# Kernel optimization log

Measured on AMD Instinct MI355X. Metric: run time of the kernel, lower is better.

Reference implementation:

```python
import jax, jax.numpy as jnp
import numpy as np

D_MODEL = 1024
N_HEADS = 16
D_K = D_MODEL // N_HEADS
SCALE = float(np.sqrt(D_K))


def setup_inputs() -> dict:
    key = jax.random.key(0)
    ks = jax.random.split(key, 8)
    B, S = 2, 2048
    init = 1.0 / np.sqrt(D_MODEL)
    return {
        "query": jax.random.normal(ks[0], (B, S, D_MODEL), dtype=jnp.float32),
        "key": jax.random.normal(ks[1], (B, S, D_MODEL), dtype=jnp.float32),
        "value": jax.random.normal(ks[2], (B, S, D_MODEL), dtype=jnp.float32),
        "w_q": jax.random.uniform(ks[3], (D_MODEL, D_MODEL), jnp.float32, -init, init),
        "w_k": jax.random.uniform(ks[4], (D_MODEL, D_MODEL), jnp.float32, -init, init),
        "w_v": jax.random.uniform(ks[5], (D_MODEL, D_MODEL), jnp.float32, -init, init),
        "w_o": jax.random.uniform(ks[6], (D_MODEL, D_MODEL), jnp.float32, -init, init),
        "b_o": jax.random.uniform(ks[7], (D_MODEL,), jnp.float32, -init, init),
    }


def reference(query, key, value, w_q, w_k, w_v, w_o, b_o):
    B, S, _ = query.shape
    # nn.Linear computes x @ W.T; weights stored torch-style [out, in]
    def proj(x, w):
        # [B,S,D] -> [B,H,S,Dk]
        return (x @ w.T).reshape(B, S, N_HEADS, D_K).transpose(0, 2, 1, 3)

    Q = proj(query, w_q)
    K = proj(key, w_k)
    V = proj(value, w_v)
    scores = jnp.einsum("bhqd,bhkd->bhqk", Q, K) / SCALE  # [B,H,S,S]
    attn = jax.nn.softmax(scores, axis=-1)
    out = jnp.einsum("bhqk,bhkd->bhqd", attn, V)  # [B,H,S,Dk]
    out = out.transpose(0, 2, 1, 3).reshape(B, S, D_MODEL)
    out = out @ w_o.T + b_o
    return (out, attn)
```

## Files before the change

kernel.cpp:

```cpp
#include <hip/hip_runtime.h>
#include <hip/hip_bf16.h>

typedef unsigned int u32;
typedef unsigned short u16;
using bf16x8 = __attribute__((ext_vector_type(8))) short;
using f32x4  = __attribute__((ext_vector_type(4))) float;

#define S_LEN 2048
#define DK 64
#define NH 16
#define DMODEL 1024
#define NROWS 4096

__device__ __forceinline__ u16 f2bf(float f){
  u32 u = __builtin_bit_cast(u32, f);
  u += 0x7fffu + ((u >> 16) & 1u);
  return (u16)(u >> 16);
}

__device__ __forceinline__ void gload_lds16(const u16* g, u16* l){
  __builtin_amdgcn_global_load_lds(
      (__attribute__((address_space(1))) u32*)(void*)const_cast<u16*>(g),
      (__attribute__((address_space(3))) u32*)(void*)l, 16, 0, 0);
}

#define TILE_BARRIER_VM4() do { \
  asm volatile("s_waitcnt vmcnt(4) lgkmcnt(0)" ::: "memory"); \
  __builtin_amdgcn_s_barrier(); \
  __builtin_amdgcn_sched_barrier(0); \
} while (0)

#define TILE_BARRIER_VM0() do { \
  asm volatile("s_waitcnt vmcnt(0) lgkmcnt(0)" ::: "memory"); \
  __builtin_amdgcn_s_barrier(); \
  __builtin_amdgcn_sched_barrier(0); \
} while (0)

__global__ void cvt_all(const float* __restrict__ q, const float* __restrict__ k,
                        const float* __restrict__ v, const float* __restrict__ wq,
                        const float* __restrict__ wk, const float* __restrict__ wv,
                        const float* __restrict__ wo, u16* __restrict__ ws)
{
  const int y = blockIdx.y;
  const int n4 = (y < 3) ? (NROWS*DMODEL/4) : (DMODEL*DMODEL/4);
  const int i = blockIdx.x * blockDim.x + threadIdx.x;
  if (i >= n4) return;
  const float* src = (y==0)?q:(y==1)?k:(y==2)?v:(y==3)?wq:(y==4)?wk:(y==5)?wv:wo;
  u16* dst = ws + ((y < 3) ? (size_t)y*(NROWS*DMODEL)
                           : (size_t)3*(NROWS*DMODEL) + (size_t)(y-3)*(DMODEL*DMODEL));
  float4 val = reinterpret_cast<const float4*>(src)[i];
  ushort4 o;
  o.x = f2bf(val.x); o.y = f2bf(val.y); o.z = f2bf(val.z); o.w = f2bf(val.w);
  reinterpret_cast<ushort4*>(dst)[i] = o;
}

template<bool OUTGEMM>
__global__ __launch_bounds__(256)
void gemm_mha(const u16* __restrict__ Abase, const u16* __restrict__ Bbase,
              u16* __restrict__ Qh, u16* __restrict__ Kh, u16* __restrict__ Vt,
              float* __restrict__ Out, const float* __restrict__ bias)
{
  __shared__ u16 smem[32768];
  u16* As = smem;
  u16* Bs = smem + 16384;

  const int tid  = threadIdx.x;
  const int lane = tid & 63;
  const int wid  = tid >> 6;
  const int lo = lane & 15, hi = lane >> 4;
  const int z = OUTGEMM ? 0 : blockIdx.z;
  const int m0 = blockIdx.x * 128;
  const int n0 = blockIdx.y * 128;
  const u16* ga = Abase + (size_t)z * (NROWS*DMODEL)  + (size_t)m0 * DMODEL;
  const u16* gb = Bbase + (size_t)z * (DMODEL*DMODEL) + (size_t)n0 * DMODEL;

  const int wm = (wid >> 1) * 64;
  const int wn = (wid & 1) * 64;

  f32x4 acc[4][4] = {};

  auto stage = [&](int buf, int kt){
    const u16* a = ga + kt * 64;
    const u16* b = gb + kt * 64;
    #pragma unroll
    for (int i = 0; i < 4; ++i){
      const int chunk = i*256 + tid;
      const int row = chunk >> 3, c8 = chunk & 7;
      gload_lds16(a + (size_t)row*DMODEL + c8*8, &As[buf*8192 + (i*256 + wid*64)*8]);
      gload_lds16(b + (size_t)row*DMODEL + c8*8, &Bs[buf*8192 + (i*256 + wid*64)*8]);
    }
  };

  stage(0, 0);
  __syncthreads();

  for (int t = 0; t < DMODEL/64; ++t){
    const int buf = t & 1;
    if (t + 1 < DMODEL/64) stage(buf ^ 1, t + 1);
    const u16* as = &As[buf*8192];
    const u16* bs = &Bs[buf*8192];
    #pragma unroll
    for (int ks = 0; ks < 2; ++ks){
      bf16x8 af[4], bfr[4];
      #pragma unroll
      for (int i = 0; i < 4; ++i){
        af[i]  = *reinterpret_cast<const bf16x8*>(&as[(wm + i*16 + lo)*64 + ks*32 + hi*8]);
        bfr[i] = *reinterpret_cast<const bf16x8*>(&bs[(wn + i*16 + lo)*64 + ks*32 + hi*8]);
      }
      #pragma unroll
      for (int mi = 0; mi < 4; ++mi)
        #pragma unroll
        for (int ni = 0; ni < 4; ++ni)
          acc[mi][ni] = __builtin_amdgcn_mfma_f32_16x16x32_bf16(af[mi], bfr[ni], acc[mi][ni], 0, 0, 0);
    }
    __syncthreads();
  }

  if constexpr (OUTGEMM){
    #pragma unroll
    for (int mi = 0; mi < 4; ++mi)
    #pragma unroll
    for (int ni = 0; ni < 4; ++ni)
    #pragma unroll
    for (int r = 0; r < 4; ++r){
      const int m = m0 + wm + mi*16 + hi*4 + r;
      const int n = n0 + wn + ni*16 + lo;
      __builtin_nontemporal_store(acc[mi][ni][r] + bias[n],
                                  &Out[(size_t)m * DMODEL + n]);
    }
  } else {
    const float scale = (z == 0) ? 0.18033688011112043f : 1.0f;
    if (z == 2){
      #pragma unroll
      for (int mi = 0; mi < 4; ++mi)
      #pragma unroll
      for (int ni = 0; ni < 4; ++ni)
      #pragma unroll
      for (int r = 0; r < 4; ++r)
        smem[(size_t)(wn + ni*16 + lo)*136 + wm + mi*16 + hi*4 + r] = f2bf(acc[mi][ni][r]);
    } else {
      #pragma unroll
      for (int mi = 0; mi < 4; ++mi)
      #pragma unroll
      for (int ni = 0; ni < 4; ++ni)
      #pragma unroll
      for (int r = 0; r < 4; ++r)
        smem[(size_t)(wm + mi*16 + hi*4 + r)*136 + wn + ni*16 + lo] = f2bf(acc[mi][ni][r] * scale);
    }
    __syncthreads();
    const int b = m0 >> 11, s0 = m0 & 2047;
    #pragma unroll
    for (int it = 0; it < 8; ++it){
      const int c = it*256 + tid;
      const int rr = c >> 4, cc = c & 15;
      bf16x8 v = *reinterpret_cast<const bf16x8*>(&smem[(size_t)rr*136 + cc*8]);
      if (z == 2){
        const int gn = n0 + rr, h = gn >> 6, d = gn & 63;
        *reinterpret_cast<bf16x8*>(&Vt[(((size_t)(b*NH + h))*DK + d)*S_LEN + s0 + cc*8]) = v;
      } else {
        const int gn = n0 + cc*8, h = gn >> 6, d0 = gn & 63;
        u16* dst = z ? Kh : Qh;
        *reinterpret_cast<bf16x8*>(&dst[(((size_t)(b*NH + h))*S_LEN + s0 + rr)*DK + d0]) = v;
      }
    }
  }
}

__global__ __launch_bounds__(512)
void attn_fused(const u16* __restrict__ Qh, const u16* __restrict__ Kh,
                const u16* __restrict__ Vt, float* __restrict__ attn,
                u16* __restrict__ ctx)
{
  constexpr int S = S_LEN;
  __shared__ u16 KV[2][2][64*64];
  __shared__ float Pf[8][16*40];

  const int tid = threadIdx.x, lane = tid & 63, w = tid >> 6;
  const int lo = lane & 15, hi = lane >> 4;

  const int idx = blockIdx.x;
  const int slot = idx >> 3;
  const int qt = slot & 15;
  const int bh = (idx & 7) + 8 * (slot >> 4);

  const int q0 = qt*128 + w*16;
  const u16* Qb = Qh + (size_t)bh * S * DK;
  const u16* Kb = Kh + (size_t)bh * S * DK;
  const u16* Vb = Vt + (size_t)bh * DK * S;
  float* attn_b = attn + (size_t)bh * S * S;

  bf16x8 aq[2];
  #pragma unroll
  for (int ks = 0; ks < 2; ++ks)
    aq[ks] = *reinterpret_cast<const bf16x8*>(
        &Qb[(size_t)(q0 + lo) * DK + ks*32 + hi*8]);

  auto qk = [&](const u16* tile, f32x4 (&s)[4]){
    #pragma unroll
    for (int ks = 0; ks < 2; ++ks){
      bf16x8 bk[4];
      #pragma unroll
      for (int kf = 0; kf < 4; ++kf){
        const int row = kf*16 + lo;
        bk[kf] = *reinterpret_cast<const bf16x8*>(
            &tile[row*64 + (((ks*4 + hi) ^ (row&7))*8)]);
      }
      #pragma unroll
      for (int kf = 0; kf < 4; ++kf)
        s[kf] = __builtin_amdgcn_mfma_f32_16x16x32_bf16(aq[ks], bk[kf], s[kf], 0, 0, 0);
    }
  };

  {
    u16* KP0 = &KV[0][0][0];
    u16* KP1 = &KV[1][0][0];
    auto stage128 = [&](u16* dst, int t16){
      const u16* kt = Kb + (size_t)t16 * 128 * DK;
      #pragma unroll
      for (int i = 0; i < 2; ++i){
        const int u_ = i*512 + tid;
        const int r = u_ >> 3, c = u_ & 7;
        gload_lds16(kt + (size_t)r*DK + ((c ^ (r&7))*8), dst + (i*512 + w*64)*8);
      }
    };
    stage128(KP0, 0);
    __syncthreads();
    float l_part[4] = {};
    for (int t = 0; t < S/128; ++t){
      u16* cur = (t & 1) ? KP1 : KP0;
      u16* nxt = (t & 1) ? KP0 : KP1;
      if (t + 1 < S/128) stage128(nxt, t + 1);
      #pragma unroll
      for (int sub = 0; sub < 2; ++sub){
        f32x4 s[4] = {};
        qk(cur + sub*4096, s);
        #pragma unroll
        for (int r = 0; r < 4; ++r)
          l_part[r] += exp2f(s[0][r]) + exp2f(s[1][r]) + exp2f(s[2][r]) + exp2f(s[3][r]);
      }
      __syncthreads();
    }
    float inv_l[4];
    #pragma unroll
    for (int r = 0; r < 4; ++r){
      float v = l_part[r];
      v += __shfl_xor(v, 1, 64);
      v += __shfl_xor(v, 2, 64);
      v += __shfl_xor(v, 4, 64);
      v += __shfl_xor(v, 8, 64);
      inv_l[r] = 1.0f / v;
    }

    const int sr = tid >> 3, sc = tid & 7;
    auto stageK = [&](int buf, int t){
      gload_lds16(Kb + (size_t)t*64*DK + (size_t)sr*DK + ((sc ^ (sr&7))*8),
                  &KV[buf][0][w*512]);
    };
    auto stageV = [&](int buf, int t){
      gload_lds16(Vb + (size_t)sr*S + t*64 + ((sc ^ (sr&7))*8),
                  &KV[buf][1][w*512]);
    };

    stageK(0, 0); stageV(0, 0);
    TILE_BARRIER_VM0();
    f32x4 o[4] = {};
    for (int t = 0; t < S/64; ++t){
      const int buf = t & 1;
      if (t + 1 < S/64){ stageK(buf ^ 1, t + 1); stageV(buf ^ 1, t + 1); }
      f32x4 s[4] = {};
      qk(&KV[buf][0][0], s);

      #pragma unroll
      for (int half = 0; half < 2; ++half){
        #pragma unroll
        for (int k2 = 0; k2 < 2; ++k2){
          const int kf = half*2 + k2;
          #pragma unroll
          for (int r = 0; r < 4; ++r){
            const int row = hi*4 + r;
            const int col = k2*16 + lo;
            Pf[w][row*40 + ((((col>>2) ^ (row&7)) << 2) | (col & 3))] =
                exp2f(s[kf][r]) * inv_l[r];
          }
        }
        #pragma unroll
        for (int j = 0; j < 2; ++j){
          const int row = j*8 + (lane >> 3);
          const int cb  = (lane & 7) * 4;
          f32x4 vv = *reinterpret_cast<const f32x4*>(
              &Pf[w][row*40 + ((((cb>>2) ^ (row&7)) << 2))]);
          __builtin_nontemporal_store(vv, reinterpret_cast<f32x4*>(
              &attn_b[(size_t)(q0 + row)*S + t*64 + half*32 + cb]));
        }
        {
          const int row = lo;
          const f32x4 pa = *reinterpret_cast<const f32x4*>(
              &Pf[w][row*40 + (((2*hi) ^ (row&7)) << 2)]);
          const f32x4 pb = *reinterpret_cast<const f32x4*>(
              &Pf[w][row*40 + (((2*hi + 1) ^ (row&7)) << 2)]);
          union { bf16x8 v; __hip_bfloat162 h[4]; } u_;
          u_.h[0] = __float22bfloat162_rn(float2{pa[0], pa[1]});
          u_.h[1] = __float22bfloat162_rn(float2{pa[2], pa[3]});
          u_.h[2] = __float22bfloat162_rn(float2{pb[0], pb[1]});
          u_.h[3] = __float22bfloat162_rn(float2{pb[2], pb[3]});
          bf16x8 bv[4];
          #pragma unroll
          for (int df = 0; df < 4; ++df){
            const int vrow = df*16 + lo;
            bv[df] = *reinterpret_cast<const bf16x8*>(
                &KV[buf][1][vrow*64 + (((half*4 + hi) ^ (vrow&7))*8)]);
          }
          #pragma unroll
          for (int df = 0; df < 4; ++df)
            o[df] = __builtin_amdgcn_mfma_f32_16x16x32_bf16(u_.v, bv[df], o[df], 0, 0, 0);
        }
      }

      if (t + 1 < S/64){
        TILE_BARRIER_VM4();
      }
    }

    const int b = bh >> 4, h = bh & 15;
    #pragma unroll
    for (int df = 0; df < 4; ++df)
    #pragma unroll
    for (int r = 0; r < 4; ++r){
      const int qq = q0 + hi*4 + r;
      const int d  = df*16 + lo;
      ctx[((size_t)b * S + qq) * DMODEL + h*DK + d] = f2bf(o[df][r]);
    }
  }
}

extern "C" void kernel_launch(void* const* d_in, const int* in_sizes, int n_in,
                              void* d_out, int out_size, void* d_ws, size_t ws_size,
                              hipStream_t stream)
{
  const float* q_in = (const float*)d_in[0];
  const float* k_in = (const float*)d_in[1];
  const float* v_in = (const float*)d_in[2];
  const float* wq   = (const float*)d_in[3];
  const float* wk   = (const float*)d_in[4];
  const float* wv   = (const float*)d_in[5];
  const float* wo   = (const float*)d_in[6];
  const float* bo   = (const float*)d_in[7];

  u16* ws = (u16*)d_ws;
  u16* X  = ws;
  u16* W  = ws + (size_t)3*NROWS*DMODEL;
  u16* Wob= W  + (size_t)3*DMODEL*DMODEL;
  u16* Qh = W  + (size_t)4*DMODEL*DMODEL;
  u16* Kh = Qh + (size_t)NROWS*DMODEL;
  u16* Vt = Kh + (size_t)NROWS*DMODEL;
  u16* Ctx= Vt + (size_t)NROWS*DMODEL;

  cvt_all<<<dim3(4096, 7), 256, 0, stream>>>(q_in, k_in, v_in, wq, wk, wv, wo, ws);

  gemm_mha<false><<<dim3(32, 8, 3), 256, 0, stream>>>(X, W, Qh, Kh, Vt, nullptr, nullptr);

  float* out0 = (float*)d_out;
  float* attn = out0 + (size_t)NROWS * DMODEL;
  attn_fused<<<dim3(512), 512, 0, stream>>>(Qh, Kh, Vt, attn, Ctx);

  gemm_mha<true><<<dim3(32, 8), 256, 0, stream>>>(Ctx, Wob, nullptr, nullptr, nullptr, out0, bo);
}
```

Baseline: 220.9 us.

## Fuse fp32-to-bf16 activation conversion into QKV projection GEMM A-tile staging

Result: slower. 226.8 us (+2.7%).

```diff
diff --git a/kernel.cpp b/kernel.cpp
--- a/kernel.cpp
+++ b/kernel.cpp
@@ -36,28 +36,135 @@
   __builtin_amdgcn_sched_barrier(0); \
 } while (0)
 
-__global__ void cvt_all(const float* __restrict__ q, const float* __restrict__ k,
-                        const float* __restrict__ v, const float* __restrict__ wq,
-                        const float* __restrict__ wk, const float* __restrict__ wv,
-                        const float* __restrict__ wo, u16* __restrict__ ws)
+__global__ void cvt_w(const float* __restrict__ wq, const float* __restrict__ wk,
+                      const float* __restrict__ wv, const float* __restrict__ wo,
+                      u16* __restrict__ dstbase)
 {
   const int y = blockIdx.y;
-  const int n4 = (y < 3) ? (NROWS*DMODEL/4) : (DMODEL*DMODEL/4);
+  const float* src = (y==0)?wq:(y==1)?wk:(y==2)?wv:wo;
+  u16* dst = dstbase + (size_t)y * (DMODEL*DMODEL);
   const int i = blockIdx.x * blockDim.x + threadIdx.x;
-  if (i >= n4) return;
-  const float* src = (y==0)?q:(y==1)?k:(y==2)?v:(y==3)?wq:(y==4)?wk:(y==5)?wv:wo;
-  u16* dst = ws + ((y < 3) ? (size_t)y*(NROWS*DMODEL)
-                           : (size_t)3*(NROWS*DMODEL) + (size_t)(y-3)*(DMODEL*DMODEL));
   float4 val = reinterpret_cast<const float4*>(src)[i];
   ushort4 o;
   o.x = f2bf(val.x); o.y = f2bf(val.y); o.z = f2bf(val.z); o.w = f2bf(val.w);
   reinterpret_cast<ushort4*>(dst)[i] = o;
 }
 
-template<bool OUTGEMM>
 __global__ __launch_bounds__(256)
-void gemm_mha(const u16* __restrict__ Abase, const u16* __restrict__ Bbase,
-              u16* __restrict__ Qh, u16* __restrict__ Kh, u16* __restrict__ Vt,
+void gemm_qkv(const float* __restrict__ qin, const float* __restrict__ kin,
+              const float* __restrict__ vin, const u16* __restrict__ Wbase,
+              u16* __restrict__ Qh, u16* __restrict__ Kh, u16* __restrict__ Vt)
+{
+  __shared__ u16 smem[32768];
+  u16* As = smem;
+  u16* Bs = smem + 16384;
+
+  const int tid  = threadIdx.x;
+  const int lane = tid & 63;
+  const int wid  = tid >> 6;
+  const int lo = lane & 15, hi = lane >> 4;
+  const int z = blockIdx.z;
+  const int m0 = blockIdx.x * 128;
+  const int n0 = blockIdx.y * 128;
+  const float* ga = ((z==0)?qin:(z==1)?kin:vin) + (size_t)m0 * DMODEL;
+  const u16*   gb = Wbase + (size_t)z * (DMODEL*DMODEL) + (size_t)n0 * DMODEL;
+
+  const int wm = (wid >> 1) * 64;
+  const int wn = (wid & 1) * 64;
+
+  f32x4 acc[4][4] = {};
+
+  auto stageA = [&](int buf, int kt){
+    const float* a = ga + kt * 64;
+    #pragma unroll
+    for (int i = 0; i < 4; ++i){
+      const int chunk = i*256 + tid;
+      const int row = chunk >> 3, c8 = chunk & 7;
+      const float* src = a + (size_t)row*DMODEL + c8*8;
+      const float4 v0 = *reinterpret_cast<const float4*>(src);
+      const float4 v1 = *reinterpret_cast<const float4*>(src + 4);
+      union { bf16x8 v; __hip_bfloat162 h[4]; } u_;
+      u_.h[0] = __float22bfloat162_rn(float2{v0.x, v0.y});
+      u_.h[1] = __float22bfloat162_rn(float2{v0.z, v0.w});
+      u_.h[2] = __float22bfloat162_rn(float2{v1.x, v1.y});
+      u_.h[3] = __float22bfloat162_rn(float2{v1.z, v1.w});
+      *reinterpret_cast<bf16x8*>(&As[buf*8192 + chunk*8]) = u_.v;
+    }
+  };
+  auto stageB = [&](int buf, int kt){
+    const u16* b = gb + kt * 64;
+    #pragma unroll
+    for (int i = 0; i < 4; ++i){
+      const int chunk = i*256 + tid;
+      const int row = chunk >> 3, c8 = chunk & 7;
+      gload_lds16(b + (size_t)row*DMODEL + c8*8, &Bs[buf*8192 + (i*256 + wid*64)*8]);
+    }
+  };
+
+  stageB(0, 0);
+  stageA(0, 0);
+  __syncthreads();
+
+  for (int t = 0; t < DMODEL/64; ++t){
+    const int buf = t & 1;
+    if (t + 1 < DMODEL/64){ stageB(buf ^ 1, t + 1); stageA(buf ^ 1, t + 1); }
+    const u16* as = &As[buf*8192];
+    const u16* bs = &Bs[buf*8192];
+    #pragma unroll
+    for (int ks = 0; ks < 2; ++ks){
+      bf16x8 af[4], bfr[4];
+      #pragma unroll
+      for (int i = 0; i < 4; ++i){
+        af[i]  = *reinterpret_cast<const bf16x8*>(&as[(wm + i*16 + lo)*64 + ks*32 + hi*8]);
+        bfr[i] = *reinterpret_cast<const bf16x8*>(&bs[(wn + i*16 + lo)*64 + ks*32 + hi*8]);
+      }
+      #pragma unroll
+      for (int mi = 0; mi < 4; ++mi)
+        #pragma unroll
+        for (int ni = 0; ni < 4; ++ni)
+          acc[mi][ni] = __builtin_amdgcn_mfma_f32_16x16x32_bf16(af[mi], bfr[ni], acc[mi][ni], 0, 0, 0);
+    }
+    __syncthreads();
+  }
+
+  const float scale = (z == 0) ? 0.18033688011112043f : 1.0f;
+  if (z == 2){
+    #pragma unroll
+    for (int mi = 0; mi < 4; ++mi)
+    #pragma unroll
+    for (int ni = 0; ni < 4; ++ni)
+    #pragma unroll
+    for (int r = 0; r < 4; ++r)
+      smem[(size_t)(wn + ni*16 + lo)*136 + wm + mi*16 + hi*4 + r] = f2bf(acc[mi][ni][r]);
+  } else {
+    #pragma unroll
+    for (int mi = 0; mi < 4; ++mi)
+    #pragma unroll
+    for (int ni = 0; ni < 4; ++ni)
+    #pragma unroll
+    for (int r = 0; r < 4; ++r)
+      smem[(size_t)(wm + mi*16 + hi*4 + r)*136 + wn + ni*16 + lo] = f2bf(acc[mi][ni][r] * scale);
+  }
+  __syncthreads();
+  const int b = m0 >> 11, s0 = m0 & 2047;
+  #pragma unroll
+  for (int it = 0; it < 8; ++it){
+    const int c = it*256 + tid;
+    const int rr = c >> 4, cc = c & 15;
+    bf16x8 v = *reinterpret_cast<const bf16x8*>(&smem[(size_t)rr*136 + cc*8]);
+    if (z == 2){
+      const int gn = n0 + rr, h = gn >> 6, d = gn & 63;
+      *reinterpret_cast<bf16x8*>(&Vt[(((size_t)(b*NH + h))*DK + d)*S_LEN + s0 + cc*8]) = v;
+    } else {
+      const int gn = n0 + cc*8, h = gn >> 6, d0 = gn & 63;
+      u16* dst = z ? Kh : Qh;
+      *reinterpret_cast<bf16x8*>(&dst[(((size_t)(b*NH + h))*S_LEN + s0 + rr)*DK + d0]) = v;
+    }
+  }
+}
+
+__global__ __launch_bounds__(256)
+void gemm_out(const u16* __restrict__ Abase, const u16* __restrict__ Bbase,
               float* __restrict__ Out, const float* __restrict__ bias)
 {
   __shared__ u16 smem[32768];
@@ -68,11 +175,10 @@
   const int lane = tid & 63;
   const int wid  = tid >> 6;
   const int lo = lane & 15, hi = lane >> 4;
-  const int z = OUTGEMM ? 0 : blockIdx.z;
   const int m0 = blockIdx.x * 128;
   const int n0 = blockIdx.y * 128;
-  const u16* ga = Abase + (size_t)z * (NROWS*DMODEL)  + (size_t)m0 * DMODEL;
-  const u16* gb = Bbase + (size_t)z * (DMODEL*DMODEL) + (size_t)n0 * DMODEL;
+  const u16* ga = Abase + (size_t)m0 * DMODEL;
+  const u16* gb = Bbase + (size_t)n0 * DMODEL;
 
   const int wm = (wid >> 1) * 64;
   const int wn = (wid & 1) * 64;
@@ -116,53 +222,16 @@
     __syncthreads();
   }
 
-  if constexpr (OUTGEMM){
-    #pragma unroll
-    for (int mi = 0; mi < 4; ++mi)
-    #pragma unroll
-    for (int ni = 0; ni < 4; ++ni)
-    #pragma unroll
-    for (int r = 0; r < 4; ++r){
-      const int m = m0 + wm + mi*16 + hi*4 + r;
-      const int n = n0 + wn + ni*16 + lo;
-      __builtin_nontemporal_store(acc[mi][ni][r] + bias[n],
-                                  &Out[(size_t)m * DMODEL + n]);
-    }
-  } else {
-    const float scale = (z == 0) ? 0.18033688011112043f : 1.0f;
-    if (z == 2){
-      #pragma unroll
-      for (int mi = 0; mi < 4; ++mi)
-      #pragma unroll
-      for (int ni = 0; ni < 4; ++ni)
-      #pragma unroll
-      for (int r = 0; r < 4; ++r)
-        smem[(size_t)(wn + ni*16 + lo)*136 + wm + mi*16 + hi*4 + r] = f2bf(acc[mi][ni][r]);
-    } else {
-      #pragma unroll
-      for (int mi = 0; mi < 4; ++mi)
-      #pragma unroll
-      for (int ni = 0; ni < 4; ++ni)
-      #pragma unroll
-      for (int r = 0; r < 4; ++r)
-        smem[(size_t)(wm + mi*16 + hi*4 + r)*136 + wn + ni*16 + lo] = f2bf(acc[mi][ni][r] * scale);
-    }
-    __syncthreads();
-    const int b = m0 >> 11, s0 = m0 & 2047;
-    #pragma unroll
-    for (int it = 0; it < 8; ++it){
-      const int c = it*256 + tid;
-      const int rr = c >> 4, cc = c & 15;
-      bf16x8 v = *reinterpret_cast<const bf16x8*>(&smem[(size_t)rr*136 + cc*8]);
-      if (z == 2){
-        const int gn = n0 + rr, h = gn >> 6, d = gn & 63;
-        *reinterpret_cast<bf16x8*>(&Vt[(((size_t)(b*NH + h))*DK + d)*S_LEN + s0 + cc*8]) = v;
-      } else {
-        const int gn = n0 + cc*8, h = gn >> 6, d0 = gn & 63;
-        u16* dst = z ? Kh : Qh;
-        *reinterpret_cast<bf16x8*>(&dst[(((size_t)(b*NH + h))*S_LEN + s0 + rr)*DK + d0]) = v;
-      }
-    }
+  #pragma unroll
+  for (int mi = 0; mi < 4; ++mi)
+  #pragma unroll
+  for (int ni = 0; ni < 4; ++ni)
+  #pragma unroll
+  for (int r = 0; r < 4; ++r){
+    const int m = m0 + wm + mi*16 + hi*4 + r;
+    const int n = n0 + wn + ni*16 + lo;
+    __builtin_nontemporal_store(acc[mi][ni][r] + bias[n],
+                                &Out[(size_t)m * DMODEL + n]);
   }
 }
 
@@ -211,125 +280,123 @@
     }
   };
 
-  {
-    u16* KP0 = &KV[0][0][0];
-    u16* KP1 = &KV[1][0][0];
-    auto stage128 = [&](u16* dst, int t16){
-      const u16* kt = Kb + (size_t)t16 * 128 * DK;
-      #pragma unroll
-      for (int i = 0; i < 2; ++i){
-        const int u_ = i*512 + tid;
-        const int r = u_ >> 3, c = u_ & 7;
-        gload_lds16(kt + (size_t)r*DK + ((c ^ (r&7))*8), dst + (i*512 + w*64)*8);
-      }
-    };
-    stage128(KP0, 0);
+  u16* KP0 = &KV[0][0][0];
+  u16* KP1 = &KV[1][0][0];
+  auto stage128 = [&](u16* dst, int t16){
+    const u16* kt = Kb + (size_t)t16 * 128 * DK;
+    #pragma unroll
+    for (int i = 0; i < 2; ++i){
+      const int u_ = i*512 + tid;
+      const int r = u_ >> 3, c = u_ & 7;
+      gload_lds16(kt + (size_t)r*DK + ((c ^ (r&7))*8), dst + (i*512 + w*64)*8);
+    }
+  };
+  stage128(KP0, 0);
+  __syncthreads();
+  float l_part[4] = {};
+  for (int t = 0; t < S/128; ++t){
+    u16* cur = (t & 1) ? KP1 : KP0;
+    u16* nxt = (t & 1) ? KP0 : KP1;
+    if (t + 1 < S/128) stage128(nxt, t + 1);
+    #pragma unroll
+    for (int sub = 0; sub < 2; ++sub){
+      f32x4 s[4] = {};
+      qk(cur + sub*4096, s);
+      #pragma unroll
+      for (int r = 0; r < 4; ++r)
+        l_part[r] += exp2f(s[0][r]) + exp2f(s[1][r]) + exp2f(s[2][r]) + exp2f(s[3][r]);
+    }
     __syncthreads();
-    float l_part[4] = {};
-    for (int t = 0; t < S/128; ++t){
-      u16* cur = (t & 1) ? KP1 : KP0;
-      u16* nxt = (t & 1) ? KP0 : KP1;
-      if (t + 1 < S/128) stage128(nxt, t + 1);
-      #pragma unroll
-      for (int sub = 0; sub < 2; ++sub){
-        f32x4 s[4] = {};
-        qk(cur + sub*4096, s);
+  }
+  float inv_l[4];
+  #pragma unroll
+  for (int r = 0; r < 4; ++r){
+    float v = l_part[r];
+    v += __shfl_xor(v, 1, 64);
+    v += __shfl_xor(v, 2, 64);
+    v += __shfl_xor(v, 4, 64);
+    v += __shfl_xor(v, 8, 64);
+    inv_l[r] = 1.0f / v;
+  }
+
+  const int sr = tid >> 3, sc = tid & 7;
+  auto stageK = [&](int buf, int t){
+    gload_lds16(Kb + (size_t)t*64*DK + (size_t)sr*DK + ((sc ^ (sr&7))*8),
+                &KV[buf][0][w*512]);
+  };
+  auto stageV = [&](int buf, int t){
+    gload_lds16(Vb + (size_t)sr*S + t*64 + ((sc ^ (sr&7))*8),
+                &KV[buf][1][w*512]);
+  };
+
+  stageK(0, 0); stageV(0, 0);
+  TILE_BARRIER_VM0();
+  f32x4 o[4] = {};
+  for (int t = 0; t < S/64; ++t){
+    const int buf = t & 1;
+    if (t + 1 < S/64){ stageK(buf ^ 1, t + 1); stageV(buf ^ 1, t + 1); }
+    f32x4 s[4] = {};
+    qk(&KV[buf][0][0], s);
+
+    #pragma unroll
+    for (int half = 0; half < 2; ++half){
+      #pragma unroll
+      for (int k2 = 0; k2 < 2; ++k2){
+        const int kf = half*2 + k2;
         #pragma unroll
-        for (int r = 0; r < 4; ++r)
-          l_part[r] += exp2f(s[0][r]) + exp2f(s[1][r]) + exp2f(s[2][r]) + exp2f(s[3][r]);
-      }
-      __syncthreads();
-    }
-    float inv_l[4];
-    #pragma unroll
-    for (int r = 0; r < 4; ++r){
-      float v = l_part[r];
-      v += __shfl_xor(v, 1, 64);
-      v += __shfl_xor(v, 2, 64);
-      v += __shfl_xor(v, 4, 64);
-      v += __shfl_xor(v, 8, 64);
-      inv_l[r] = 1.0f / v;
-    }
-
-    const int sr = tid >> 3, sc = tid & 7;
-    auto stageK = [&](int buf, int t){
-      gload_lds16(Kb + (size_t)t*64*DK + (size_t)sr*DK + ((sc ^ (sr&7))*8),
-                  &KV[buf][0][w*512]);
-    };
-    auto stageV = [&](int buf, int t){
-      gload_lds16(Vb + (size_t)sr*S + t*64 + ((sc ^ (sr&7))*8),
-                  &KV[buf][1][w*512]);
-    };
-
-    stageK(0, 0); stageV(0, 0);
-    TILE_BARRIER_VM0();
-    f32x4 o[4] = {};
-    for (int t = 0; t < S/64; ++t){
-      const int buf = t & 1;
-      if (t + 1 < S/64){ stageK(buf ^ 1, t + 1); stageV(buf ^ 1, t + 1); }
-      f32x4 s[4] = {};
-      qk(&KV[buf][0][0], s);
-
-      #pragma unroll
-      for (int half = 0; half < 2; ++half){
+        for (int r = 0; r < 4; ++r){
+          const int row = hi*4 + r;
+          const int col = k2*16 + lo;
+          Pf[w][row*40 + ((((col>>2) ^ (row&7)) << 2) | (col & 3))] =
+              exp2f(s[kf][r]) * inv_l[r];
+        }
+      }
+      #pragma unroll
+      for (int j = 0; j < 2; ++j){
+        const int row = j*8 + (lane >> 3);
+        const int cb  = (lane & 7) * 4;
+        f32x4 vv = *reinterpret_cast<const f32x4*>(
+            &Pf[w][row*40 + ((((cb>>2) ^ (row&7)) << 2))]);
+        __builtin_nontemporal_store(vv, reinterpret_cast<f32x4*>(
+            &attn_b[(size_t)(q0 + row)*S + t*64 + half*32 + cb]));
+      }
+      {
+        const int row = lo;
+        const f32x4 pa = *reinterpret_cast<const f32x4*>(
+            &Pf[w][row*40 + (((2*hi) ^ (row&7)) << 2)]);
+        const f32x4 pb = *reinterpret_cast<const f32x4*>(
+            &Pf[w][row*40 + (((2*hi + 1) ^ (row&7)) << 2)]);
+        union { bf16x8 v; __hip_bfloat162 h[4]; } u_;
+        u_.h[0] = __float22bfloat162_rn(float2{pa[0], pa[1]});
+        u_.h[1] = __float22bfloat162_rn(float2{pa[2], pa[3]});
+        u_.h[2] = __float22bfloat162_rn(float2{pb[0], pb[1]});
+        u_.h[3] = __float22bfloat162_rn(float2{pb[2], pb[3]});
+        bf16x8 bv[4];
         #pragma unroll
-        for (int k2 = 0; k2 < 2; ++k2){
-          const int kf = half*2 + k2;
-          #pragma unroll
-          for (int r = 0; r < 4; ++r){
-            const int row = hi*4 + r;
-            const int col = k2*16 + lo;
-            Pf[w][row*40 + ((((col>>2) ^ (row&7)) << 2) | (col & 3))] =
-                exp2f(s[kf][r]) * inv_l[r];
-          }
+        for (int df = 0; df < 4; ++df){
+          const int vrow = df*16 + lo;
+          bv[df] = *reinterpret_cast<const bf16x8*>(
+              &KV[buf][1][vrow*64 + (((half*4 + hi) ^ (vrow&7))*8)]);
         }
         #pragma unroll
-        for (int j = 0; j < 2; ++j){
-          const int row = j*8 + (lane >> 3);
-          const int cb  = (lane & 7) * 4;
-          f32x4 vv = *reinterpret_cast<const f32x4*>(
-              &Pf[w][row*40 + ((((cb>>2) ^ (row&7)) << 2))]);
-          __builtin_nontemporal_store(vv, reinterpret_cast<f32x4*>(
-              &attn_b[(size_t)(q0 + row)*S + t*64 + half*32 + cb]));
-        }
-        {
-          const int row = lo;
-          const f32x4 pa = *reinterpret_cast<const f32x4*>(
-              &Pf[w][row*40 + (((2*hi) ^ (row&7)) << 2)]);
-          const f32x4 pb = *reinterpret_cast<const f32x4*>(
-              &Pf[w][row*40 + (((2*hi + 1) ^ (row&7)) << 2)]);
-          union { bf16x8 v; __hip_bfloat162 h[4]; } u_;
-          u_.h[0] = __float22bfloat162_rn(float2{pa[0], pa[1]});
-          u_.h[1] = __float22bfloat162_rn(float2{pa[2], pa[3]});
-          u_.h[2] = __float22bfloat162_rn(float2{pb[0], pb[1]});
-          u_.h[3] = __float22bfloat162_rn(float2{pb[2], pb[3]});
-          bf16x8 bv[4];
-          #pragma unroll
-          for (int df = 0; df < 4; ++df){
-            const int vrow = df*16 + lo;
-            bv[df] = *reinterpret_cast<const bf16x8*>(
-                &KV[buf][1][vrow*64 + (((half*4 + hi) ^ (vrow&7))*8)]);
-          }
-          #pragma unroll
-          for (int df = 0; df < 4; ++df)
-            o[df] = __builtin_amdgcn_mfma_f32_16x16x32_bf16(u_.v, bv[df], o[df], 0, 0, 0);
-        }
-      }
-
-      if (t + 1 < S/64){
-        TILE_BARRIER_VM4();
-      }
-    }
-
-    const int b = bh >> 4, h = bh & 15;
-    #pragma unroll
-    for (int df = 0; df < 4; ++df)
-    #pragma unroll
-    for (int r = 0; r < 4; ++r){
-      const int qq = q0 + hi*4 + r;
-      const int d  = df*16 + lo;
-      ctx[((size_t)b * S + qq) * DMODEL + h*DK + d] = f2bf(o[df][r]);
-    }
+        for (int df = 0; df < 4; ++df)
+          o[df] = __builtin_amdgcn_mfma_f32_16x16x32_bf16(u_.v, bv[df], o[df], 0, 0, 0);
+      }
+    }
+
+    if (t + 1 < S/64){
+      TILE_BARRIER_VM4();
+    }
+  }
+
+  const int b = bh >> 4, h = bh & 15;
+  #pragma unroll
+  for (int df = 0; df < 4; ++df)
+  #pragma unroll
+  for (int r = 0; r < 4; ++r){
+    const int qq = q0 + hi*4 + r;
+    const int d  = df*16 + lo;
+    ctx[((size_t)b * S + qq) * DMODEL + h*DK + d] = f2bf(o[df][r]);
   }
 }
 
@@ -347,21 +414,19 @@
   const float* bo   = (const float*)d_in[7];
 
   u16* ws = (u16*)d_ws;
-  u16* X  = ws;
-  u16* W  = ws + (size_t)3*NROWS*DMODEL;
-  u16* Wob= W  + (size_t)3*DMODEL*DMODEL;
+  u16* W  = ws;
   u16* Qh = W  + (size_t)4*DMODEL*DMODEL;
   u16* Kh = Qh + (size_t)NROWS*DMODEL;
   u16* Vt = Kh + (size_t)NROWS*DMODEL;
   u16* Ctx= Vt + (size_t)NROWS*DMODEL;
 
-  cvt_all<<<dim3(4096, 7), 256, 0, stream>>>(q_in, k_in, v_in, wq, wk, wv, wo, ws);
-
-  gemm_mha<false><<<dim3(32, 8, 3), 256, 0, stream>>>(X, W, Qh, Kh, Vt, nullptr, nullptr);
+  cvt_w<<<dim3(1024, 4), 256, 0, stream>>>(wq, wk, wv, wo, W);
+
+  gemm_qkv<<<dim3(32, 8, 3), 256, 0, stream>>>(q_in, k_in, v_in, W, Qh, Kh, Vt);
 
   float* out0 = (float*)d_out;
   float* attn = out0 + (size_t)NROWS * DMODEL;
   attn_fused<<<dim3(512), 512, 0, stream>>>(Qh, Kh, Vt, attn, Ctx);
 
-  gemm_mha<true><<<dim3(32, 8), 256, 0, stream>>>(Ctx, Wob, nullptr, nullptr, nullptr, out0, bo);
-}
+  gemm_out<<<dim3(32, 8), 256, 0, stream>>>(Ctx, W + (size_t)3*DMODEL*DMODEL, out0, bo);
+}
```

## Triple-buffer pass-1 K staging and vectorize ctx store through LDS

Applied to the files above, without the earlier changes.

Result: no change. 221.6 us (+0.3%).

```diff
diff --git a/kernel.cpp b/kernel.cpp
--- a/kernel.cpp
+++ b/kernel.cpp
@@ -24,14 +24,8 @@
       (__attribute__((address_space(3))) u32*)(void*)l, 16, 0, 0);
 }
 
-#define TILE_BARRIER_VM4() do { \
-  asm volatile("s_waitcnt vmcnt(4) lgkmcnt(0)" ::: "memory"); \
-  __builtin_amdgcn_s_barrier(); \
-  __builtin_amdgcn_sched_barrier(0); \
-} while (0)
-
-#define TILE_BARRIER_VM0() do { \
-  asm volatile("s_waitcnt vmcnt(0) lgkmcnt(0)" ::: "memory"); \
+#define BARRIER_VM(N) do { \
+  asm volatile("s_waitcnt vmcnt(" #N ") lgkmcnt(0)" ::: "memory"); \
   __builtin_amdgcn_s_barrier(); \
   __builtin_amdgcn_sched_barrier(0); \
 } while (0)
@@ -172,11 +166,11 @@
                 u16* __restrict__ ctx)
 {
   constexpr int S = S_LEN;
-  __shared__ u16 KV[2][2][64*64];
-  __shared__ float Pf[8][16*40];
+  __shared__ u16 SM[26624];
 
   const int tid = threadIdx.x, lane = tid & 63, w = tid >> 6;
   const int lo = lane & 15, hi = lane >> 4;
+  float* Pf = (float*)(SM + 16384);
 
   const int idx = blockIdx.x;
   const int slot = idx >> 3;
@@ -211,124 +205,134 @@
     }
   };
 
-  {
-    u16* KP0 = &KV[0][0][0];
-    u16* KP1 = &KV[1][0][0];
-    auto stage128 = [&](u16* dst, int t16){
-      const u16* kt = Kb + (size_t)t16 * 128 * DK;
-      #pragma unroll
-      for (int i = 0; i < 2; ++i){
-        const int u_ = i*512 + tid;
-        const int r = u_ >> 3, c = u_ & 7;
-        gload_lds16(kt + (size_t)r*DK + ((c ^ (r&7))*8), dst + (i*512 + w*64)*8);
-      }
-    };
-    stage128(KP0, 0);
-    __syncthreads();
-    float l_part[4] = {};
-    for (int t = 0; t < S/128; ++t){
-      u16* cur = (t & 1) ? KP1 : KP0;
-      u16* nxt = (t & 1) ? KP0 : KP1;
-      if (t + 1 < S/128) stage128(nxt, t + 1);
-      #pragma unroll
-      for (int sub = 0; sub < 2; ++sub){
-        f32x4 s[4] = {};
-        qk(cur + sub*4096, s);
+  auto stage128 = [&](u16* dst, int t16){
+    const u16* kt = Kb + (size_t)t16 * 128 * DK;
+    #pragma unroll
+    for (int i = 0; i < 2; ++i){
+      const int u_ = i*512 + tid;
+      const int r = u_ >> 3, c = u_ & 7;
+      gload_lds16(kt + (size_t)r*DK + ((c ^ (r&7))*8), dst + (i*512 + w*64)*8);
+    }
+  };
+  auto p1buf = [&](int i){ return SM + (size_t)(i % 3) * 8192; };
+
+  stage128(p1buf(0), 0);
+  stage128(p1buf(1), 1);
+  BARRIER_VM(2);
+  float l_part[4] = {};
+  for (int t = 0; t < S/128; ++t){
+    if (t + 2 < S/128) stage128(p1buf(t + 2), t + 2);
+    const u16* cur = p1buf(t);
+    #pragma unroll
+    for (int sub = 0; sub < 2; ++sub){
+      f32x4 s[4] = {};
+      qk(cur + sub*4096, s);
+      #pragma unroll
+      for (int r = 0; r < 4; ++r)
+        l_part[r] += exp2f(s[0][r]) + exp2f(s[1][r]) + exp2f(s[2][r]) + exp2f(s[3][r]);
+    }
+    if (t < S/128 - 1){
+      if (t < S/128 - 2) { BARRIER_VM(2); }
+      else               { BARRIER_VM(0); }
+    }
+  }
+  float inv_l[4];
+  #pragma unroll
+  for (int r = 0; r < 4; ++r){
+    float v = l_part[r];
+    v += __shfl_xor(v, 1, 64);
+    v += __shfl_xor(v, 2, 64);
+    v += __shfl_xor(v, 4, 64);
+    v += __shfl_xor(v, 8, 64);
+    inv_l[r] = 1.0f / v;
+  }
+  BARRIER_VM(0);
+
+  const int sr = tid >> 3, sc = tid & 7;
+  auto stageK = [&](int buf, int t){
+    gload_lds16(Kb + (size_t)t*64*DK + (size_t)sr*DK + ((sc ^ (sr&7))*8),
+                SM + buf*8192 + w*512);
+  };
+  auto stageV = [&](int buf, int t){
+    gload_lds16(Vb + (size_t)sr*S + t*64 + ((sc ^ (sr&7))*8),
+                SM + buf*8192 + 4096 + w*512);
+  };
+
+  stageK(0, 0); stageV(0, 0);
+  BARRIER_VM(0);
+  f32x4 o[4] = {};
+  for (int t = 0; t < S/64; ++t){
+    const int buf = t & 1;
+    if (t + 1 < S/64){ stageK(buf ^ 1, t + 1); stageV(buf ^ 1, t + 1); }
+    f32x4 s[4] = {};
+    qk(SM + buf*8192, s);
+
+    #pragma unroll
+    for (int half = 0; half < 2; ++half){
+      #pragma unroll
+      for (int k2 = 0; k2 < 2; ++k2){
+        const int kf = half*2 + k2;
         #pragma unroll
-        for (int r = 0; r < 4; ++r)
-          l_part[r] += exp2f(s[0][r]) + exp2f(s[1][r]) + exp2f(s[2][r]) + exp2f(s[3][r]);
-      }
-      __syncthreads();
-    }
-    float inv_l[4];
-    #pragma unroll
-    for (int r = 0; r < 4; ++r){
-      float v = l_part[r];
-      v += __shfl_xor(v, 1, 64);
-      v += __shfl_xor(v, 2, 64);
-      v += __shfl_xor(v, 4, 64);
-      v += __shfl_xor(v, 8, 64);
-      inv_l[r] = 1.0f / v;
-    }
-
-    const int sr = tid >> 3, sc = tid & 7;
-    auto stageK = [&](int buf, int t){
-      gload_lds16(Kb + (size_t)t*64*DK + (size_t)sr*DK + ((sc ^ (sr&7))*8),
-                  &KV[buf][0][w*512]);
-    };
-    auto stageV = [&](int buf, int t){
-      gload_lds16(Vb + (size_t)sr*S + t*64 + ((sc ^ (sr&7))*8),
-                  &KV[buf][1][w*512]);
-    };
-
-    stageK(0, 0); stageV(0, 0);
-    TILE_BARRIER_VM0();
-    f32x4 o[4] = {};
-    for (int t = 0; t < S/64; ++t){
-      const int buf = t & 1;
-      if (t + 1 < S/64){ stageK(buf ^ 1, t + 1); stageV(buf ^ 1, t + 1); }
-      f32x4 s[4] = {};
-      qk(&KV[buf][0][0], s);
-
-      #pragma unroll
-      for (int half = 0; half < 2; ++half){
+        for (int r = 0; r < 4; ++r){
+          const int row = hi*4 + r;
+          const int col = k2*16 + lo;
+          Pf[w*640 + row*40 + ((((col>>2) ^ (row&7)) << 2) | (col & 3))] =
+              exp2f(s[kf][r]) * inv_l[r];
+        }
+      }
+      #pragma unroll
+      for (int j = 0; j < 2; ++j){
+        const int row = j*8 + (lane >> 3);
+        const int cb  = (lane & 7) * 4;
+        f32x4 vv = *reinterpret_cast<const f32x4*>(
+            &Pf[w*640 + row*40 + ((((cb>>2) ^ (row&7)) << 2))]);
+        __builtin_nontemporal_store(vv, reinterpret_cast<f32x4*>(
+            &attn_b[(size_t)(q0 + row)*S + t*64 + half*32 + cb]));
+      }
+      {
+        const int row = lo;
+        const f32x4 pa = *reinterpret_cast<const f32x4*>(
+            &Pf[w*640 + row*40 + (((2*hi) ^ (row&7)) << 2)]);
+        const f32x4 pb = *reinterpret_cast<const f32x4*>(
+            &Pf[w*640 + row*40 + (((2*hi + 1) ^ (row&7)) << 2)]);
+        union { bf16x8 v; __hip_bfloat162 h[4]; } u_;
+        u_.h[0] = __float22bfloat162_rn(float2{pa[0], pa[1]});
+        u_.h[1] = __float22bfloat162_rn(float2{pa[2], pa[3]});
+        u_.h[2] = __float22bfloat162_rn(float2{pb[0], pb[1]});
+        u_.h[3] = __float22bfloat162_rn(float2{pb[2], pb[3]});
+        bf16x8 bv[4];
         #pragma unroll
-        for (int k2 = 0; k2 < 2; ++k2){
-          const int kf = half*2 + k2;
-          #pragma unroll
-          for (int r = 0; r < 4; ++r){
-            const int row = hi*4 + r;
-            const int col = k2*16 + lo;
-            Pf[w][row*40 + ((((col>>2) ^ (row&7)) << 2) | (col & 3))] =
-                exp2f(s[kf][r]) * inv_l[r];
-          }
+        for (int df = 0; df < 4; ++df){
+          const int vrow = df*16 + lo;
+          bv[df] = *reinterpret_cast<const bf16x8*>(
+              &SM[buf*8192 + 4096 + vrow*64 + (((half*4 + hi) ^ (vrow&7))*8)]);
         }
         #pragma unroll
-        for (int j = 0; j < 2; ++j){
-          const int row = j*8 + (lane >> 3);
-          const int cb  = (lane & 7) * 4;
-          f32x4 vv = *reinterpret_cast<const f32x4*>(
-              &Pf[w][row*40 + ((((cb>>2) ^ (row&7)) << 2))]);
-          __builtin_nontemporal_store(vv, reinterpret_cast<f32x4*>(
-              &attn_b[(size_t)(q0 + row)*S + t*64 + half*32 + cb]));
-        }
-        {
-          const int row = lo;
-          const f32x4 pa = *reinterpret_cast<const f32x4*>(
-              &Pf[w][row*40 + (((2*hi) ^ (row&7)) << 2)]);
-          const f32x4 pb = *reinterpret_cast<const f32x4*>(
-              &Pf[w][row*40 + (((2*hi + 1) ^ (row&7)) << 2)]);
-          union { bf16x8 v; __hip_bfloat162 h[4]; } u_;
-          u_.h[0] = __float22bfloat162_rn(float2{pa[0], pa[1]});
-          u_.h[1] = __float22bfloat162_rn(float2{pa[2], pa[3]});
-          u_.h[2] = __float22bfloat162_rn(float2{pb[0], pb[1]});
-          u_.h[3] = __float22bfloat162_rn(float2{pb[2], pb[3]});
-          bf16x8 bv[4];
-          #pragma unroll
-          for (int df = 0; df < 4; ++df){
-            const int vrow = df*16 + lo;
-            bv[df] = *reinterpret_cast<const bf16x8*>(
-                &KV[buf][1][vrow*64 + (((half*4 + hi) ^ (vrow&7))*8)]);
-          }
-          #pragma unroll
-          for (int df = 0; df < 4; ++df)
-            o[df] = __builtin_amdgcn_mfma_f32_16x16x32_bf16(u_.v, bv[df], o[df], 0, 0, 0);
-        }
-      }
-
-      if (t + 1 < S/64){
-        TILE_BARRIER_VM4();
-      }
-    }
-
+        for (int df = 0; df < 4; ++df)
+          o[df] = __builtin_amdgcn_mfma_f32_16x16x32_bf16(u_.v, bv[df], o[df], 0, 0, 0);
+      }
+    }
+
+    if (t + 1 < S/64){
+      BARRIER_VM(4);
+    }
+  }
+
+  {
+    u16* Pw = (u16*)(Pf + (size_t)w * 640);
+    #pragma unroll
+    for (int df = 0; df < 4; ++df)
+      #pragma unroll
+      for (int r = 0; r < 4; ++r)
+        Pw[(hi*4 + r)*64 + df*16 + lo] = f2bf(o[df][r]);
     const int b = bh >> 4, h = bh & 15;
     #pragma unroll
-    for (int df = 0; df < 4; ++df)
-    #pragma unroll
-    for (int r = 0; r < 4; ++r){
-      const int qq = q0 + hi*4 + r;
-      const int d  = df*16 + lo;
-      ctx[((size_t)b * S + qq) * DMODEL + h*DK + d] = f2bf(o[df][r]);
+    for (int i = 0; i < 2; ++i){
+      const int c = i*64 + lane;
+      const int row = c >> 3, d0 = (c & 7) * 8;
+      bf16x8 v = *reinterpret_cast<const bf16x8*>(&Pw[row*64 + d0]);
+      *reinterpret_cast<bf16x8*>(
+          &ctx[((size_t)b*S + q0 + row)*DMODEL + h*DK + d0]) = v;
     }
   }
 }
```

## Halve attention block size, give each wave two query groups with overlapped passes

Applied to the files above, without the earlier changes.

New measurement: 224.7 us. No clear change (+1.7%).

```diff
diff --git a/kernel.cpp b/kernel.cpp
--- a/kernel.cpp
+++ b/kernel.cpp
@@ -24,14 +24,8 @@
       (__attribute__((address_space(3))) u32*)(void*)l, 16, 0, 0);
 }
 
-#define TILE_BARRIER_VM4() do { \
-  asm volatile("s_waitcnt vmcnt(4) lgkmcnt(0)" ::: "memory"); \
-  __builtin_amdgcn_s_barrier(); \
-  __builtin_amdgcn_sched_barrier(0); \
-} while (0)
-
-#define TILE_BARRIER_VM0() do { \
-  asm volatile("s_waitcnt vmcnt(0) lgkmcnt(0)" ::: "memory"); \
+#define BARRIER_VM(N) do { \
+  asm volatile("s_waitcnt vmcnt(" #N ") lgkmcnt(0)" ::: "memory"); \
   __builtin_amdgcn_s_barrier(); \
   __builtin_amdgcn_sched_barrier(0); \
 } while (0)
@@ -166,14 +160,14 @@
   }
 }
 
-__global__ __launch_bounds__(512)
+__global__ __launch_bounds__(256)
 void attn_fused(const u16* __restrict__ Qh, const u16* __restrict__ Kh,
                 const u16* __restrict__ Vt, float* __restrict__ attn,
                 u16* __restrict__ ctx)
 {
   constexpr int S = S_LEN;
-  __shared__ u16 KV[2][2][64*64];
-  __shared__ float Pf[8][16*40];
+  __shared__ u16 KV[2][2][4096];
+  __shared__ float Pf[4][640];
 
   const int tid = threadIdx.x, lane = tid & 63, w = tid >> 6;
   const int lo = lane & 15, hi = lane >> 4;
@@ -183,19 +177,21 @@
   const int qt = slot & 15;
   const int bh = (idx & 7) + 8 * (slot >> 4);
 
-  const int q0 = qt*128 + w*16;
+  const int q0 = qt*128 + w*32;
   const u16* Qb = Qh + (size_t)bh * S * DK;
   const u16* Kb = Kh + (size_t)bh * S * DK;
   const u16* Vb = Vt + (size_t)bh * DK * S;
   float* attn_b = attn + (size_t)bh * S * S;
 
-  bf16x8 aq[2];
+  bf16x8 aq[2][2];
   #pragma unroll
-  for (int ks = 0; ks < 2; ++ks)
-    aq[ks] = *reinterpret_cast<const bf16x8*>(
-        &Qb[(size_t)(q0 + lo) * DK + ks*32 + hi*8]);
-
-  auto qk = [&](const u16* tile, f32x4 (&s)[4]){
+  for (int g = 0; g < 2; ++g)
+    #pragma unroll
+    for (int ks = 0; ks < 2; ++ks)
+      aq[g][ks] = *reinterpret_cast<const bf16x8*>(
+          &Qb[(size_t)(q0 + g*16 + lo) * DK + ks*32 + hi*8]);
+
+  auto qk = [&](const u16* tile, const bf16x8 (&a)[2], f32x4 (&s)[4]){
     #pragma unroll
     for (int ks = 0; ks < 2; ++ks){
       bf16x8 bk[4];
@@ -207,130 +203,163 @@
       }
       #pragma unroll
       for (int kf = 0; kf < 4; ++kf)
-        s[kf] = __builtin_amdgcn_mfma_f32_16x16x32_bf16(aq[ks], bk[kf], s[kf], 0, 0, 0);
-    }
-  };
-
-  {
-    u16* KP0 = &KV[0][0][0];
-    u16* KP1 = &KV[1][0][0];
-    auto stage128 = [&](u16* dst, int t16){
-      const u16* kt = Kb + (size_t)t16 * 128 * DK;
-      #pragma unroll
-      for (int i = 0; i < 2; ++i){
-        const int u_ = i*512 + tid;
-        const int r = u_ >> 3, c = u_ & 7;
-        gload_lds16(kt + (size_t)r*DK + ((c ^ (r&7))*8), dst + (i*512 + w*64)*8);
-      }
-    };
-    stage128(KP0, 0);
-    __syncthreads();
-    float l_part[4] = {};
-    for (int t = 0; t < S/128; ++t){
-      u16* cur = (t & 1) ? KP1 : KP0;
-      u16* nxt = (t & 1) ? KP0 : KP1;
-      if (t + 1 < S/128) stage128(nxt, t + 1);
-      #pragma unroll
-      for (int sub = 0; sub < 2; ++sub){
-        f32x4 s[4] = {};
-        qk(cur + sub*4096, s);
-        #pragma unroll
-        for (int r = 0; r < 4; ++r)
-          l_part[r] += exp2f(s[0][r]) + exp2f(s[1][r]) + exp2f(s[2][r]) + exp2f(s[3][r]);
-      }
-      __syncthreads();
-    }
-    float inv_l[4];
+        s[kf] = __builtin_amdgcn_mfma_f32_16x16x32_bf16(a[ks], bk[kf], s[kf], 0, 0, 0);
+    }
+  };
+
+  auto reduce_inv = [&](float (&lp)[4], float (&inv)[4]){
     #pragma unroll
     for (int r = 0; r < 4; ++r){
-      float v = l_part[r];
+      float v = lp[r];
       v += __shfl_xor(v, 1, 64);
       v += __shfl_xor(v, 2, 64);
       v += __shfl_xor(v, 4, 64);
       v += __shfl_xor(v, 8, 64);
-      inv_l[r] = 1.0f / v;
-    }
-
-    const int sr = tid >> 3, sc = tid & 7;
-    auto stageK = [&](int buf, int t){
-      gload_lds16(Kb + (size_t)t*64*DK + (size_t)sr*DK + ((sc ^ (sr&7))*8),
-                  &KV[buf][0][w*512]);
-    };
-    auto stageV = [&](int buf, int t){
-      gload_lds16(Vb + (size_t)sr*S + t*64 + ((sc ^ (sr&7))*8),
-                  &KV[buf][1][w*512]);
-    };
-
-    stageK(0, 0); stageV(0, 0);
-    TILE_BARRIER_VM0();
-    f32x4 o[4] = {};
-    for (int t = 0; t < S/64; ++t){
-      const int buf = t & 1;
-      if (t + 1 < S/64){ stageK(buf ^ 1, t + 1); stageV(buf ^ 1, t + 1); }
+      inv[r] = 1.0f / v;
+    }
+  };
+
+  auto stage128 = [&](u16* dst, int t16){
+    const u16* kt = Kb + (size_t)t16 * 128 * DK;
+    #pragma unroll
+    for (int i = 0; i < 4; ++i){
+      const int u_ = i*256 + tid;
+      const int r = u_ >> 3, c = u_ & 7;
+      gload_lds16(kt + (size_t)r*DK + ((c ^ (r&7))*8), dst + (i*256 + w*64)*8);
+    }
+  };
+  stage128(&KV[0][0][0], 0);
+  __syncthreads();
+  float l0p[4] = {};
+  for (int t = 0; t < S/128; ++t){
+    if (t + 1 < S/128) stage128(&KV[(t+1)&1][0][0], t + 1);
+    const u16* cur = &KV[t&1][0][0];
+    #pragma unroll
+    for (int sub = 0; sub < 2; ++sub){
       f32x4 s[4] = {};
-      qk(&KV[buf][0][0], s);
-
-      #pragma unroll
-      for (int half = 0; half < 2; ++half){
+      qk(cur + sub*4096, aq[0], s);
+      #pragma unroll
+      for (int r = 0; r < 4; ++r)
+        l0p[r] += exp2f(s[0][r]) + exp2f(s[1][r]) + exp2f(s[2][r]) + exp2f(s[3][r]);
+    }
+    if (t < S/128 - 1) __syncthreads();
+  }
+  float inv_l0[4];
+  reduce_inv(l0p, inv_l0);
+
+  auto stageK = [&](int buf, int t){
+    #pragma unroll
+    for (int i = 0; i < 2; ++i){
+      const int u_ = i*256 + tid;
+      const int r = u_ >> 3, c = u_ & 7;
+      gload_lds16(Kb + (size_t)t*64*DK + (size_t)r*DK + ((c ^ (r&7))*8),
+                  &KV[buf][0][(i*256 + w*64)*8]);
+    }
+  };
+  auto stageV = [&](int buf, int t){
+    #pragma unroll
+    for (int i = 0; i < 2; ++i){
+      const int u_ = i*256 + tid;
+      const int r = u_ >> 3, c = u_ & 7;
+      gload_lds16(Vb + (size_t)r*S + t*64 + ((c ^ (r&7))*8),
+                  &KV[buf][1][(i*256 + w*64)*8]);
+    }
+  };
+
+  auto store_pv = [&](int buf, int t, const f32x4 (&s)[4], const float (&inv_l)[4],
+                      int g, f32x4 (&o)[4]){
+    const int qg = q0 + g*16;
+    #pragma unroll
+    for (int half = 0; half < 2; ++half){
+      #pragma unroll
+      for (int k2 = 0; k2 < 2; ++k2){
+        const int kf = half*2 + k2;
         #pragma unroll
-        for (int k2 = 0; k2 < 2; ++k2){
-          const int kf = half*2 + k2;
-          #pragma unroll
-          for (int r = 0; r < 4; ++r){
-            const int row = hi*4 + r;
-            const int col = k2*16 + lo;
-            Pf[w][row*40 + ((((col>>2) ^ (row&7)) << 2) | (col & 3))] =
-                exp2f(s[kf][r]) * inv_l[r];
-          }
+        for (int r = 0; r < 4; ++r){
+          const int row = hi*4 + r;
+          const int col = k2*16 + lo;
+          Pf[w][row*40 + ((((col>>2) ^ (row&7)) << 2) | (col & 3))] =
+              exp2f(s[kf][r]) * inv_l[r];
+        }
+      }
+      #pragma unroll
+      for (int j = 0; j < 2; ++j){
+        const int row = j*8 + (lane >> 3);
+        const int cb  = (lane & 7) * 4;
+        f32x4 vv = *reinterpret_cast<const f32x4*>(
+            &Pf[w][row*40 + ((((cb>>2) ^ (row&7)) << 2))]);
+        __builtin_nontemporal_store(vv, reinterpret_cast<f32x4*>(
+            &attn_b[(size_t)(qg + row)*S + t*64 + half*32 + cb]));
+      }
+      {
+        const int row = lo;
+        const f32x4 pa = *reinterpret_cast<const f32x4*>(
+            &Pf[w][row*40 + (((2*hi) ^ (row&7)) << 2)]);
+        const f32x4 pb = *reinterpret_cast<const f32x4*>(
+            &Pf[w][row*40 + (((2*hi + 1) ^ (row&7)) << 2)]);
+        union { bf16x8 v; __hip_bfloat162 h[4]; } u_;
+        u_.h[0] = __float22bfloat162_rn(float2{pa[0], pa[1]});
+        u_.h[1] = __float22bfloat162_rn(float2{pa[2], pa[3]});
+        u_.h[2] = __float22bfloat162_rn(float2{pb[0], pb[1]});
+        u_.h[3] = __float22bfloat162_rn(float2{pb[2], pb[3]});
+        bf16x8 bv[4];
+        #pragma unroll
+        for (int df = 0; df < 4; ++df){
+          const int vrow = df*16 + lo;
+          bv[df] = *reinterpret_cast<const bf16x8*>(
+              &KV[buf][1][vrow*64 + (((half*4 + hi) ^ (vrow&7))*8)]);
         }
         #pragma unroll
-        for (int j = 0; j < 2; ++j){
-          const int row = j*8 + (lane >> 3);
-          const int cb  = (lane & 7) * 4;
-          f32x4 vv = *reinterpret_cast<const f32x4*>(
-              &Pf[w][row*40 + ((((cb>>2) ^ (row&7)) << 2))]);
-          __builtin_nontemporal_store(vv, reinterpret_cast<f32x4*>(
-              &attn_b[(size_t)(q0 + row)*S + t*64 + half*32 + cb]));
-        }
-        {
-          const int row = lo;
-          const f32x4 pa = *reinterpret_cast<const f32x4*>(
-              &Pf[w][row*40 + (((2*hi) ^ (row&7)) << 2)]);
-          const f32x4 pb = *reinterpret_cast<const f32x4*>(
-              &Pf[w][row*40 + (((2*hi + 1) ^ (row&7)) << 2)]);
-          union { bf16x8 v; __hip_bfloat162 h[4]; } u_;
-          u_.h[0] = __float22bfloat162_rn(float2{pa[0], pa[1]});
-          u_.h[1] = __float22bfloat162_rn(float2{pa[2], pa[3]});
-          u_.h[2] = __float22bfloat162_rn(float2{pb[0], pb[1]});
-          u_.h[3] = __float22bfloat162_rn(float2{pb[2], pb[3]});
-          bf16x8 bv[4];
-          #pragma unroll
-          for (int df = 0; df < 4; ++df){
-            const int vrow = df*16 + lo;
-            bv[df] = *reinterpret_cast<const bf16x8*>(
-                &KV[buf][1][vrow*64 + (((half*4 + hi) ^ (vrow&7))*8)]);
-          }
-          #pragma unroll
-          for (int df = 0; df < 4; ++df)
-            o[df] = __builtin_amdgcn_mfma_f32_16x16x32_bf16(u_.v, bv[df], o[df], 0, 0, 0);
-        }
-      }
-
-      if (t + 1 < S/64){
-        TILE_BARRIER_VM4();
-      }
-    }
-
-    const int b = bh >> 4, h = bh & 15;
+        for (int df = 0; df < 4; ++df)
+          o[df] = __builtin_amdgcn_mfma_f32_16x16x32_bf16(u_.v, bv[df], o[df], 0, 0, 0);
+      }
+    }
+  };
+
+  stageK(0, 0); stageV(0, 0);
+  BARRIER_VM(0);
+  f32x4 o0[4] = {};
+  float l1p[4] = {};
+  for (int t = 0; t < S/64; ++t){
+    const int buf = t & 1;
+    if (t + 1 < S/64){ stageK(buf ^ 1, t + 1); stageV(buf ^ 1, t + 1); }
+    f32x4 s[4] = {};
+    qk(&KV[buf][0][0], aq[0], s);
+    store_pv(buf, t, s, inv_l0, 0, o0);
+    f32x4 s1[4] = {};
+    qk(&KV[buf][0][0], aq[1], s1);
+    #pragma unroll
+    for (int r = 0; r < 4; ++r)
+      l1p[r] += exp2f(s1[0][r]) + exp2f(s1[1][r]) + exp2f(s1[2][r]) + exp2f(s1[3][r]);
+    if (t + 1 < S/64) BARRIER_VM(4);
+  }
+  float inv_l1[4];
+  reduce_inv(l1p, inv_l1);
+
+  stageK(0, 0); stageV(0, 0);
+  BARRIER_VM(0);
+  f32x4 o1[4] = {};
+  for (int t = 0; t < S/64; ++t){
+    const int buf = t & 1;
+    if (t + 1 < S/64){ stageK(buf ^ 1, t + 1); stageV(buf ^ 1, t + 1); }
+    f32x4 s[4] = {};
+    qk(&KV[buf][0][0], aq[1], s);
+    store_pv(buf, t, s, inv_l1, 1, o1);
+    if (t + 1 < S/64) BARRIER_VM(4);
+  }
+
+  const int b = bh >> 4, h = bh & 15;
+  #pragma unroll
+  for (int g = 0; g < 2; ++g)
     #pragma unroll
     for (int df = 0; df < 4; ++df)
-    #pragma unroll
-    for (int r = 0; r < 4; ++r){
-      const int qq = q0 + hi*4 + r;
-      const int d  = df*16 + lo;
-      ctx[((size_t)b * S + qq) * DMODEL + h*DK + d] = f2bf(o[df][r]);
-    }
-  }
+      #pragma unroll
+      for (int r = 0; r < 4; ++r){
+        const int qq = q0 + g*16 + hi*4 + r;
+        const int d  = df*16 + lo;
+        const float vv = g ? o1[df][r] : o0[df][r];
+        ctx[((size_t)b * S + qq) * DMODEL + h*DK + d] = f2bf(vv);
+      }
 }
 
 extern "C" void kernel_launch(void* const* d_in, const int* in_sizes, int n_in,
@@ -361,7 +390,7 @@
 
   float* out0 = (float*)d_out;
   float* attn = out0 + (size_t)NROWS * DMODEL;
-  attn_fused<<<dim3(512), 512, 0, stream>>>(Qh, Kh, Vt, attn, Ctx);
+  attn_fused<<<dim3(512), 256, 0, stream>>>(Qh, Kh, Vt, attn, Ctx);
 
   gemm_mha<true><<<dim3(32, 8), 256, 0, stream>>>(Ctx, Wob, nullptr, nullptr, nullptr, out0, bo);
 }
```
